# Optimization experiments

Measured on AMD Instinct MI355X. Metric: run time of the kernel, lower is better.

## Reference

```python
import jax, jax.numpy as jnp
import numpy as np

B, C, H, W = 8, 256, 128, 128
QK = 64

def setup_inputs() -> dict:
    key = jax.random.key(0)
    ks = jax.random.split(key, 8)
    s = 0.02
    return {
        "x": jax.random.normal(ks[0], (B, C, H, W), dtype=jnp.float32),
        "wq": jax.random.normal(ks[1], (QK, C), dtype=jnp.float32) * s,
        "bq": jax.random.normal(ks[2], (QK,), dtype=jnp.float32) * s,
        "wk": jax.random.normal(ks[3], (QK, C), dtype=jnp.float32) * s,
        "bk": jax.random.normal(ks[4], (QK,), dtype=jnp.float32) * s,
        "wv": jax.random.normal(ks[5], (C, C), dtype=jnp.float32) * s,
        "bv": jax.random.normal(ks[6], (C,), dtype=jnp.float32) * s,
        "gamma": jax.random.normal(ks[7], (1,), dtype=jnp.float32) * 0.1,
    }

def reference(x, wq, bq, wk, bk, wv, bv, gamma):
    # 1x1 convs == per-pixel linear projections over channels
    Q = jnp.einsum('bchw,oc->bohw', x, wq) + bq[None, :, None, None]  # (b,qk,h,w)
    K = jnp.einsum('bchw,oc->bohw', x, wk) + bk[None, :, None, None]  # (b,qk,h,w)
    V = jnp.einsum('bchw,oc->bohw', x, wv) + bv[None, :, None, None]  # (b,c,h,w)
    # row attention: for each (b,h) row, scores over width pairs
    scores = jnp.einsum('bchw,bchv->bhwv', Q, K)          # (b,h,w_q,w_k)
    attn = jax.nn.softmax(scores, axis=-1)                # softmax over keys (dim=2 after bmm)
    out = jnp.einsum('bchv,bhwv->bchw', V, attn)          # (b,c,h,w)
    return gamma[0] * out + x
```

## Files before the change

### kernel.cpp

```cpp
#include <hip/hip_runtime.h>
#include <hip/hip_bf16.h>


typedef short bf16x8 __attribute__((ext_vector_type(8)));
typedef float f32x4 __attribute__((ext_vector_type(4)));
using u32 = unsigned int;
using u16 = unsigned short;

#define XT_OFF   0
#define XT_SB    528
#define QT_OFF   67584
#define KT_OFF   86016
#define QK_SB    144
#define PL_OFF   67584
#define PL_SB    272
#define WP_OFF   104448
#define VL_OFF   141312
#define VL_SB    272
#define SMP_OFF  141312
#define BIAS_OFF 158720
#define LDS_TOTAL 160256

#define WS_WQK   0
#define WS_WV    73728

__device__ __forceinline__ u16 bfbits(float f) {
    __hip_bfloat16 h = __float2bfloat16(f);
    u16 u; __builtin_memcpy(&u, &h, 2); return u;
}
__device__ __forceinline__ u32 packbf2(float a, float b) {
    return (u32)bfbits(a) | ((u32)bfbits(b) << 16);
}
__device__ __forceinline__ float bf2f(u16 u) {
    union { u32 i; float f; } v; v.i = ((u32)u) << 16; return v.f;
}

__device__ __forceinline__ void gl2lds16(const char* g, const char* l) {
    __builtin_amdgcn_global_load_lds(
        (const __attribute__((address_space(1))) void*)(unsigned long long)g,
        (__attribute__((address_space(3))) void*)(u32)(unsigned long long)l,
        16, 0, 0);
}
__device__ __forceinline__ void stage18k(const char* g, const char* lds, int w, int l) {
    gl2lds16(g + w * 1024 + l * 16, lds + w * 1024);
    if (l < 8) gl2lds16(g + 16384 + w * 128 + l * 16, lds + 16384 + w * 128);
}
__device__ __forceinline__ void stage36k(const char* g, const char* lds, int w, int l) {
    gl2lds16(g + w * 1024 + l * 16,         lds + w * 1024);
    gl2lds16(g + 16384 + w * 1024 + l * 16, lds + 16384 + w * 1024);
    if (l < 16) gl2lds16(g + 32768 + w * 256 + l * 16, lds + 32768 + w * 256);
}

#define GATE(WAITSTR) do { \
    __builtin_amdgcn_sched_barrier(0); \
    asm volatile(WAITSTR "\n\ts_barrier" ::: "memory"); \
    __builtin_amdgcn_sched_barrier(0); \
} while (0)

__device__ __forceinline__ void hard_barrier() {
    __builtin_amdgcn_sched_barrier(0);
    asm volatile("s_barrier" ::: "memory");
    __builtin_amdgcn_sched_barrier(0);
}
__device__ __forceinline__ void lgkm_barrier() {
    __builtin_amdgcn_sched_barrier(0);
    asm volatile("s_waitcnt lgkmcnt(0)\n\ts_barrier" ::: "memory");
    __builtin_amdgcn_sched_barrier(0);
}
__device__ __forceinline__ void pin() { __builtin_amdgcn_sched_barrier(0); }

__global__ void prep_weights(const float* __restrict__ wq, const float* __restrict__ wk,
                             const float* __restrict__ wv, u32* __restrict__ ws) {
    int i = blockIdx.x * 256 + threadIdx.x;
    if (i >= 55296) return;
    u32 v = 0;
    if (i < 18432) {
        int c = i / 2304, rem = i % 2304;
        int row = rem / 36, iw = rem % 36;
        int kc = c >> 1;
        const float* m = (c & 1) ? wk : wq;
        if (iw < 32) {
            int col = kc * 64 + iw * 2;
            v = packbf2(m[row * 256 + col], m[row * 256 + col + 1]);
        }
    } else {
        int j = i - 18432;
        int c = j / 2304, rem = j % 2304;
        int row = rem / 36, iw = rem % 36;
        int mc = c >> 2, kc = c & 3;
        if (iw < 32) {
            int col = kc * 64 + iw * 2;
            v = packbf2(wv[(mc * 64 + row) * 256 + col], wv[(mc * 64 + row) * 256 + col + 1]);
        }
    }
    ws[i] = v;
}

__global__ __launch_bounds__(1024, 4) void rowattn_mfma(
    const float* __restrict__ x,
    const float* __restrict__ bq,
    const float* __restrict__ bk,
    const float* __restrict__ bv,
    const float* __restrict__ gamma,
    const char* __restrict__ wsp,
    float* __restrict__ out)
{
    __shared__ __align__(16) char smem[LDS_TOTAL];
    const int t  = threadIdx.x;
    const int l  = t & 63;
    const int a  = l & 15;
    const int q  = l >> 4;
    const int wid = __builtin_amdgcn_readfirstlane(t >> 6);
    const int mi = wid >> 2;
    const int nj = wid & 3;
    const int w0 = nj * 32;

    const int blk = blockIdx.x;
    const int b   = blk >> 5;
    const int h0  = (blk & 31) * 4;

    const char* wqk_g = wsp + WS_WQK;
    const char* wv_g  = wsp + WS_WV;
    const float g = gamma[0];

    stage18k(wqk_g,         smem + WP_OFF,         wid, l);
    stage18k(wqk_g + 18432, smem + WP_OFF + 18432, wid, l);
    pin();

    float* biasl = (float*)(smem + BIAS_OFF);
    if (t < 384) {
        float v;
        if (t < 64) v = bq[t];
        else if (t < 128) v = bk[t - 64];
        else v = bv[t - 128];
        biasl[t] = v;
    }

    const int xw  = ((wid & 8) << 3) + l;
    const int xcb = (wid & 7) * 4;
    const float* xbase = x + (size_t)(b * 256 + xcb) * 16384 + xw;
    float xv[32];
    {
        const float* xp = xbase + h0 * 128;
#pragma unroll
        for (int p = 0; p < 8; ++p)
#pragma unroll
            for (int j = 0; j < 4; ++j)
                xv[p * 4 + j] = xp[(p * 32 + j) * 16384];
    }
    pin();

#pragma unroll 1
    for (int r = 0; r < 4; ++r) {
        const int h = h0 + r;
        if (r) lgkm_barrier();

#pragma unroll
        for (int p = 0; p < 8; ++p) {
            uint2 pk;
            pk.x = packbf2(xv[p * 4 + 0], xv[p * 4 + 1]);
            pk.y = packbf2(xv[p * 4 + 2], xv[p * 4 + 3]);
            *(uint2*)(smem + XT_OFF + xw * XT_SB + (xcb + p * 32) * 2) = pk;
        }
        GATE("s_waitcnt vmcnt(8) lgkmcnt(0)");

        f32x4 accQ[2], accK[2];
        {
            f32x4 cq, ck;
#pragma unroll
            for (int rr = 0; rr < 4; ++rr) {
                cq[rr] = biasl[mi * 16 + q * 4 + rr];
                ck[rr] = biasl[64 + mi * 16 + q * 4 + rr];
            }
            accQ[0] = cq; accQ[1] = cq; accK[0] = ck; accK[1] = ck;
        }
#pragma unroll
        for (int kc = 0; kc < 4; ++kc) {
            if (kc == 2) GATE("s_waitcnt vmcnt(2)");
            if (kc == 3) GATE("s_waitcnt vmcnt(0)");
            const char* wqp = smem + WP_OFF + (kc & 1) * 18432;
            const char* wkp = wqp + 9216;
#pragma unroll
            for (int ks = 0; ks < 2; ++ks) {
                bf16x8 aq = *(const bf16x8*)(wqp + (mi * 16 + a) * 144 + ks * 64 + q * 16);
                bf16x8 ak = *(const bf16x8*)(wkp + (mi * 16 + a) * 144 + ks * 64 + q * 16);
#pragma unroll
                for (int nt = 0; nt < 2; ++nt) {
                    bf16x8 bx = *(const bf16x8*)(smem + XT_OFF + (w0 + nt * 16 + a) * XT_SB + (kc * 64 + ks * 32) * 2 + q * 16);
                    accQ[nt] = __builtin_amdgcn_mfma_f32_16x16x32_bf16(aq, bx, accQ[nt], 0, 0, 0);
                    accK[nt] = __builtin_amdgcn_mfma_f32_16x16x32_bf16(ak, bx, accK[nt], 0, 0, 0);
                }
            }
            if (kc == 0) { hard_barrier(); stage18k(wqk_g + 2 * 18432, smem + WP_OFF,         wid, l); pin(); }
            if (kc == 1) { hard_barrier(); stage18k(wqk_g + 3 * 18432, smem + WP_OFF + 18432, wid, l); pin(); }
        }
#pragma unroll
        for (int nt = 0; nt < 2; ++nt) {
            const int wrow = w0 + nt * 16 + a;
            uint2 pq; pq.x = packbf2(accQ[nt][0], accQ[nt][1]); pq.y = packbf2(accQ[nt][2], accQ[nt][3]);
            *(uint2*)(smem + QT_OFF + wrow * QK_SB + (mi * 16 + q * 4) * 2) = pq;
            uint2 pk; pk.x = packbf2(accK[nt][0], accK[nt][1]); pk.y = packbf2(accK[nt][2], accK[nt][3]);
            *(uint2*)(smem + KT_OFF + wrow * QK_SB + (mi * 16 + q * 4) * 2) = pk;
        }
        GATE("s_waitcnt lgkmcnt(0)");
        stage36k(wv_g, smem + WP_OFF, wid, l);
        pin();

        f32x4 st[2][2];
#pragma unroll
        for (int mt2 = 0; mt2 < 2; ++mt2)
#pragma unroll
            for (int nt = 0; nt < 2; ++nt) st[mt2][nt] = (f32x4){0.f, 0.f, 0.f, 0.f};
#pragma unroll
        for (int ks = 0; ks < 2; ++ks) {
            bf16x8 bq0 = *(const bf16x8*)(smem + QT_OFF + (w0 + a) * QK_SB + ks * 64 + q * 16);
            bf16x8 bq1 = *(const bf16x8*)(smem + QT_OFF + (w0 + 16 + a) * QK_SB + ks * 64 + q * 16);
            bf16x8 ak0 = *(const bf16x8*)(smem + KT_OFF + (mi * 32 + a) * QK_SB + ks * 64 + q * 16);
            bf16x8 ak1 = *(const bf16x8*)(smem + KT_OFF + (mi * 32 + 16 + a) * QK_SB + ks * 64 + q * 16);
            st[0][0] = __builtin_amdgcn_mfma_f32_16x16x32_bf16(ak0, bq0, st[0][0], 0, 0, 0);
            st[0][1] = __builtin_amdgcn_mfma_f32_16x16x32_bf16(ak0, bq1, st[0][1], 0, 0, 0);
            st[1][0] = __builtin_amdgcn_mfma_f32_16x16x32_bf16(ak1, bq0, st[1][0], 0, 0, 0);
            st[1][1] = __builtin_amdgcn_mfma_f32_16x16x32_bf16(ak1, bq1, st[1][1], 0, 0, 0);
        }
        {
            float pmax[2], psum[2];
#pragma unroll
            for (int nt = 0; nt < 2; ++nt) {
                float mx = -3.0e38f;
#pragma unroll
                for (int mt2 = 0; mt2 < 2; ++mt2)
#pragma unroll
                    for (int rr = 0; rr < 4; ++rr) mx = fmaxf(mx, st[mt2][nt][rr]);
                mx = fmaxf(mx, __shfl_xor(mx, 16, 64));
                mx = fmaxf(mx, __shfl_xor(mx, 32, 64));
                float s = 0.f;
#pragma unroll
                for (int mt2 = 0; mt2 < 2; ++mt2)
#pragma unroll
                    for (int rr = 0; rr < 4; ++rr) {
                        float e = __expf(st[mt2][nt][rr] - mx); st[mt2][nt][rr] = e; s += e;
                    }
                s += __shfl_xor(s, 16, 64);
                s += __shfl_xor(s, 32, 64);
                pmax[nt] = mx; psum[nt] = s;
            }
            float2* smp = (float2*)(smem + SMP_OFF);
            if (q == 0) {
#pragma unroll
                for (int nt = 0; nt < 2; ++nt)
                    smp[(w0 + nt * 16 + a) * 4 + mi] = make_float2(pmax[nt], psum[nt]);
            }
            lgkm_barrier();
            float f[2];
#pragma unroll
            for (int nt = 0; nt < 2; ++nt) {
                const int wq = w0 + nt * 16 + a;
                float2 pp0 = smp[wq * 4 + 0], pp1 = smp[wq * 4 + 1];
                float2 pp2 = smp[wq * 4 + 2], pp3 = smp[wq * 4 + 3];
                float m = fmaxf(fmaxf(pp0.x, pp1.x), fmaxf(pp2.x, pp3.x));
                float s = pp0.y * __expf(pp0.x - m) + pp1.y * __expf(pp1.x - m)
                        + pp2.y * __expf(pp2.x - m) + pp3.y * __expf(pp3.x - m);
                f[nt] = __expf(pmax[nt] - m) / s;
            }
#pragma unroll
            for (int nt = 0; nt < 2; ++nt) {
                const int wq = w0 + nt * 16 + a;
#pragma unroll
                for (int mt2 = 0; mt2 < 2; ++mt2) {
                    uint2 pp;
                    pp.x = packbf2(st[mt2][nt][0] * f[nt], st[mt2][nt][1] * f[nt]);
                    pp.y = packbf2(st[mt2][nt][2] * f[nt], st[mt2][nt][3] * f[nt]);
                    *(uint2*)(smem + PL_OFF + wq * PL_SB + (mi * 32 + mt2 * 16 + q * 4) * 2) = pp;
                }
            }
        }

#pragma unroll 1
        for (int mc = 0; mc < 4; ++mc) {
            if (mc == 0)              GATE("s_waitcnt vmcnt(0) lgkmcnt(0)");
            else if (mc < 3)          GATE("s_waitcnt vmcnt(8) lgkmcnt(0)");
            else if (r < 3)           GATE("s_waitcnt vmcnt(40) lgkmcnt(0)");
            else                      GATE("s_waitcnt vmcnt(8) lgkmcnt(0)");
            f32x4 accV[2];
            {
                f32x4 cv;
#pragma unroll
                for (int rr = 0; rr < 4; ++rr) cv[rr] = biasl[128 + mc * 64 + mi * 16 + q * 4 + rr];
                accV[0] = cv; accV[1] = cv;
            }
#pragma unroll
            for (int kc = 0; kc < 4; ++kc) {
                const char* wvp = smem + WP_OFF + kc * 9216;
#pragma unroll
                for (int ks = 0; ks < 2; ++ks) {
                    bf16x8 av = *(const bf16x8*)(wvp + (mi * 16 + a) * 144 + ks * 64 + q * 16);
#pragma unroll
                    for (int nt = 0; nt < 2; ++nt) {
                        bf16x8 bx = *(const bf16x8*)(smem + XT_OFF + (w0 + nt * 16 + a) * XT_SB + (kc * 64 + ks * 32) * 2 + q * 16);
                        accV[nt] = __builtin_amdgcn_mfma_f32_16x16x32_bf16(av, bx, accV[nt], 0, 0, 0);
                    }
                }
            }
#pragma unroll
            for (int nt = 0; nt < 2; ++nt)
#pragma unroll
                for (int rr = 0; rr < 4; ++rr)
                    *(u16*)(smem + VL_OFF + (mi * 16 + q * 4 + rr) * VL_SB + (w0 + nt * 16 + a) * 2) = bfbits(accV[nt][rr]);
            GATE("s_waitcnt lgkmcnt(0)");
            if (mc < 3) {
                stage36k(wv_g + (mc + 1) * 36864, smem + WP_OFF, wid, l);
                pin();
                if (mc == 2 && r < 3) {
                    const float* xn = xbase + (h + 1) * 128;
#pragma unroll
                    for (int p = 0; p < 8; ++p)
#pragma unroll
                        for (int j = 0; j < 4; ++j)
                            xv[p * 4 + j] = xn[(p * 32 + j) * 16384];
                    pin();
                }
            } else if (r < 3) {
                stage18k(wqk_g,         smem + WP_OFF,         wid, l);
                stage18k(wqk_g + 18432, smem + WP_OFF + 18432, wid, l);
                pin();
            }
            f32x4 accO[2];
            accO[0] = (f32x4){0.f, 0.f, 0.f, 0.f};
            accO[1] = (f32x4){0.f, 0.f, 0.f, 0.f};
#pragma unroll
            for (int ks = 0; ks < 4; ++ks) {
                bf16x8 av = *(const bf16x8*)(smem + VL_OFF + (mi * 16 + a) * VL_SB + ks * 64 + q * 16);
#pragma unroll
                for (int nt = 0; nt < 2; ++nt) {
                    bf16x8 bp = *(const bf16x8*)(smem + PL_OFF + (w0 + nt * 16 + a) * PL_SB + ks * 64 + q * 16);
                    accO[nt] = __builtin_amdgcn_mfma_f32_16x16x32_bf16(av, bp, accO[nt], 0, 0, 0);
                }
            }
            uint2 xp4[2];
#pragma unroll
            for (int nt = 0; nt < 2; ++nt)
                xp4[nt] = *(const uint2*)(smem + XT_OFF + (w0 + nt * 16 + a) * XT_SB + (mc * 64 + mi * 16 + q * 4) * 2);
#pragma unroll
            for (int rr = 0; rr < 4; ++rr) {
                const int c = mc * 64 + mi * 16 + q * 4 + rr;
                float* orow = out + ((b * 256 + c) * 128 + h) * 128;
#pragma unroll
                for (int nt = 0; nt < 2; ++nt) {
                    const int w = w0 + nt * 16 + a;
                    u32 word = (rr & 2) ? xp4[nt].y : xp4[nt].x;
                    u16 xvr = (rr & 1) ? (u16)(word >> 16) : (u16)(word & 0xffff);
                    orow[w] = g * accO[nt][rr] + bf2f(xvr);
                }
            }
        }
    }
}

extern "C" void kernel_launch(void* const* d_in, const int* in_sizes, int n_in,
                              void* d_out, int out_size, void* d_ws, size_t ws_size,
                              hipStream_t stream) {
    const float* x     = (const float*)d_in[0];
    const float* wq    = (const float*)d_in[1];
    const float* bq    = (const float*)d_in[2];
    const float* wk    = (const float*)d_in[3];
    const float* bk    = (const float*)d_in[4];
    const float* wv    = (const float*)d_in[5];
    const float* bv    = (const float*)d_in[6];
    const float* gamma = (const float*)d_in[7];
    float* out = (float*)d_out;

    hipLaunchKernelGGL(prep_weights, dim3(216), dim3(256), 0, stream, wq, wk, wv, (u32*)d_ws);
    hipLaunchKernelGGL(rowattn_mfma, dim3(256), dim3(1024), 0, stream,
                       x, bq, bk, bv, gamma, (const char*)d_ws, out);
}
```

Before: 359.8 us.

## Launch one block per image row instead of four pipelined rows per block

New measurement: 295.4 us. 17.9% less time.

```diff
diff --git a/kernel.cpp b/kernel.cpp
--- a/kernel.cpp
+++ b/kernel.cpp
@@ -96,7 +96,7 @@
     ws[i] = v;
 }
 
-__global__ __launch_bounds__(1024, 4) void rowattn_mfma(
+__global__ __launch_bounds__(1024, 1) void rowattn_mfma(
     const float* __restrict__ x,
     const float* __restrict__ bq,
     const float* __restrict__ bk,
@@ -115,9 +115,9 @@
     const int nj = wid & 3;
     const int w0 = nj * 32;
 
-    const int blk = blockIdx.x;
-    const int b   = blk >> 5;
-    const int h0  = (blk & 31) * 4;
+    const int bh = blockIdx.x;
+    const int b  = bh >> 7;
+    const int h  = bh & 127;
 
     const char* wqk_g = wsp + WS_WQK;
     const char* wv_g  = wsp + WS_WV;
@@ -135,35 +135,29 @@
         else v = bv[t - 128];
         biasl[t] = v;
     }
+    pin();
 
     const int xw  = ((wid & 8) << 3) + l;
     const int xcb = (wid & 7) * 4;
-    const float* xbase = x + (size_t)(b * 256 + xcb) * 16384 + xw;
+    const float* xp = x + (size_t)(b * 256 + xcb) * 16384 + (size_t)h * 128 + xw;
     float xv[32];
+#pragma unroll
+    for (int p = 0; p < 8; ++p)
+#pragma unroll
+        for (int j = 0; j < 4; ++j)
+            xv[p * 4 + j] = xp[(p * 32 + j) * 16384];
+    pin();
+
+#pragma unroll
+    for (int p = 0; p < 8; ++p) {
+        uint2 pk;
+        pk.x = packbf2(xv[p * 4 + 0], xv[p * 4 + 1]);
+        pk.y = packbf2(xv[p * 4 + 2], xv[p * 4 + 3]);
+        *(uint2*)(smem + XT_OFF + xw * XT_SB + (xcb + p * 32) * 2) = pk;
+    }
+    GATE("s_waitcnt lgkmcnt(0)");
+
     {
-        const float* xp = xbase + h0 * 128;
-#pragma unroll
-        for (int p = 0; p < 8; ++p)
-#pragma unroll
-            for (int j = 0; j < 4; ++j)
-                xv[p * 4 + j] = xp[(p * 32 + j) * 16384];
-    }
-    pin();
-
-#pragma unroll 1
-    for (int r = 0; r < 4; ++r) {
-        const int h = h0 + r;
-        if (r) lgkm_barrier();
-
-#pragma unroll
-        for (int p = 0; p < 8; ++p) {
-            uint2 pk;
-            pk.x = packbf2(xv[p * 4 + 0], xv[p * 4 + 1]);
-            pk.y = packbf2(xv[p * 4 + 2], xv[p * 4 + 3]);
-            *(uint2*)(smem + XT_OFF + xw * XT_SB + (xcb + p * 32) * 2) = pk;
-        }
-        GATE("s_waitcnt vmcnt(8) lgkmcnt(0)");
-
         f32x4 accQ[2], accK[2];
         {
             f32x4 cq, ck;
@@ -202,155 +196,140 @@
             uint2 pk; pk.x = packbf2(accK[nt][0], accK[nt][1]); pk.y = packbf2(accK[nt][2], accK[nt][3]);
             *(uint2*)(smem + KT_OFF + wrow * QK_SB + (mi * 16 + q * 4) * 2) = pk;
         }
+    }
+    GATE("s_waitcnt lgkmcnt(0)");
+    stage36k(wv_g, smem + WP_OFF, wid, l);
+    pin();
+
+    f32x4 st[2][2];
+#pragma unroll
+    for (int mt2 = 0; mt2 < 2; ++mt2)
+#pragma unroll
+        for (int nt = 0; nt < 2; ++nt) st[mt2][nt] = (f32x4){0.f, 0.f, 0.f, 0.f};
+#pragma unroll
+    for (int ks = 0; ks < 2; ++ks) {
+        bf16x8 bq0 = *(const bf16x8*)(smem + QT_OFF + (w0 + a) * QK_SB + ks * 64 + q * 16);
+        bf16x8 bq1 = *(const bf16x8*)(smem + QT_OFF + (w0 + 16 + a) * QK_SB + ks * 64 + q * 16);
+        bf16x8 ak0 = *(const bf16x8*)(smem + KT_OFF + (mi * 32 + a) * QK_SB + ks * 64 + q * 16);
+        bf16x8 ak1 = *(const bf16x8*)(smem + KT_OFF + (mi * 32 + 16 + a) * QK_SB + ks * 64 + q * 16);
+        st[0][0] = __builtin_amdgcn_mfma_f32_16x16x32_bf16(ak0, bq0, st[0][0], 0, 0, 0);
+        st[0][1] = __builtin_amdgcn_mfma_f32_16x16x32_bf16(ak0, bq1, st[0][1], 0, 0, 0);
+        st[1][0] = __builtin_amdgcn_mfma_f32_16x16x32_bf16(ak1, bq0, st[1][0], 0, 0, 0);
+        st[1][1] = __builtin_amdgcn_mfma_f32_16x16x32_bf16(ak1, bq1, st[1][1], 0, 0, 0);
+    }
+    {
+        float pmax[2], psum[2];
+#pragma unroll
+        for (int nt = 0; nt < 2; ++nt) {
+            float mx = -3.0e38f;
+#pragma unroll
+            for (int mt2 = 0; mt2 < 2; ++mt2)
+#pragma unroll
+                for (int rr = 0; rr < 4; ++rr) mx = fmaxf(mx, st[mt2][nt][rr]);
+            mx = fmaxf(mx, __shfl_xor(mx, 16, 64));
+            mx = fmaxf(mx, __shfl_xor(mx, 32, 64));
+            float s = 0.f;
+#pragma unroll
+            for (int mt2 = 0; mt2 < 2; ++mt2)
+#pragma unroll
+                for (int rr = 0; rr < 4; ++rr) {
+                    float e = __expf(st[mt2][nt][rr] - mx); st[mt2][nt][rr] = e; s += e;
+                }
+            s += __shfl_xor(s, 16, 64);
+            s += __shfl_xor(s, 32, 64);
+            pmax[nt] = mx; psum[nt] = s;
+        }
+        float2* smp = (float2*)(smem + SMP_OFF);
+        if (q == 0) {
+#pragma unroll
+            for (int nt = 0; nt < 2; ++nt)
+                smp[(w0 + nt * 16 + a) * 4 + mi] = make_float2(pmax[nt], psum[nt]);
+        }
+        lgkm_barrier();
+        float f[2];
+#pragma unroll
+        for (int nt = 0; nt < 2; ++nt) {
+            const int wq = w0 + nt * 16 + a;
+            float2 pp0 = smp[wq * 4 + 0], pp1 = smp[wq * 4 + 1];
+            float2 pp2 = smp[wq * 4 + 2], pp3 = smp[wq * 4 + 3];
+            float m = fmaxf(fmaxf(pp0.x, pp1.x), fmaxf(pp2.x, pp3.x));
+            float s = pp0.y * __expf(pp0.x - m) + pp1.y * __expf(pp1.x - m)
+                    + pp2.y * __expf(pp2.x - m) + pp3.y * __expf(pp3.x - m);
+            f[nt] = __expf(pmax[nt] - m) / s;
+        }
+#pragma unroll
+        for (int nt = 0; nt < 2; ++nt) {
+            const int wq = w0 + nt * 16 + a;
+#pragma unroll
+            for (int mt2 = 0; mt2 < 2; ++mt2) {
+                uint2 pp;
+                pp.x = packbf2(st[mt2][nt][0] * f[nt], st[mt2][nt][1] * f[nt]);
+                pp.y = packbf2(st[mt2][nt][2] * f[nt], st[mt2][nt][3] * f[nt]);
+                *(uint2*)(smem + PL_OFF + wq * PL_SB + (mi * 32 + mt2 * 16 + q * 4) * 2) = pp;
+            }
+        }
+    }
+
+#pragma unroll 1
+    for (int mc = 0; mc < 4; ++mc) {
+        if (mc == 0) GATE("s_waitcnt vmcnt(0) lgkmcnt(0)");
+        else         GATE("s_waitcnt vmcnt(8) lgkmcnt(0)");
+        f32x4 accV[2];
+        {
+            f32x4 cv;
+#pragma unroll
+            for (int rr = 0; rr < 4; ++rr) cv[rr] = biasl[128 + mc * 64 + mi * 16 + q * 4 + rr];
+            accV[0] = cv; accV[1] = cv;
+        }
+#pragma unroll
+        for (int kc = 0; kc < 4; ++kc) {
+            const char* wvp = smem + WP_OFF + kc * 9216;
+#pragma unroll
+            for (int ks = 0; ks < 2; ++ks) {
+                bf16x8 av = *(const bf16x8*)(wvp + (mi * 16 + a) * 144 + ks * 64 + q * 16);
+#pragma unroll
+                for (int nt = 0; nt < 2; ++nt) {
+                    bf16x8 bx = *(const bf16x8*)(smem + XT_OFF + (w0 + nt * 16 + a) * XT_SB + (kc * 64 + ks * 32) * 2 + q * 16);
+                    accV[nt] = __builtin_amdgcn_mfma_f32_16x16x32_bf16(av, bx, accV[nt], 0, 0, 0);
+                }
+            }
+        }
+#pragma unroll
+        for (int nt = 0; nt < 2; ++nt)
+#pragma unroll
+            for (int rr = 0; rr < 4; ++rr)
+                *(u16*)(smem + VL_OFF + (mi * 16 + q * 4 + rr) * VL_SB + (w0 + nt * 16 + a) * 2) = bfbits(accV[nt][rr]);
         GATE("s_waitcnt lgkmcnt(0)");
-        stage36k(wv_g, smem + WP_OFF, wid, l);
-        pin();
-
-        f32x4 st[2][2];
-#pragma unroll
-        for (int mt2 = 0; mt2 < 2; ++mt2)
-#pragma unroll
-            for (int nt = 0; nt < 2; ++nt) st[mt2][nt] = (f32x4){0.f, 0.f, 0.f, 0.f};
-#pragma unroll
-        for (int ks = 0; ks < 2; ++ks) {
-            bf16x8 bq0 = *(const bf16x8*)(smem + QT_OFF + (w0 + a) * QK_SB + ks * 64 + q * 16);
-            bf16x8 bq1 = *(const bf16x8*)(smem + QT_OFF + (w0 + 16 + a) * QK_SB + ks * 64 + q * 16);
-            bf16x8 ak0 = *(const bf16x8*)(smem + KT_OFF + (mi * 32 + a) * QK_SB + ks * 64 + q * 16);
-            bf16x8 ak1 = *(const bf16x8*)(smem + KT_OFF + (mi * 32 + 16 + a) * QK_SB + ks * 64 + q * 16);
-            st[0][0] = __builtin_amdgcn_mfma_f32_16x16x32_bf16(ak0, bq0, st[0][0], 0, 0, 0);
-            st[0][1] = __builtin_amdgcn_mfma_f32_16x16x32_bf16(ak0, bq1, st[0][1], 0, 0, 0);
-            st[1][0] = __builtin_amdgcn_mfma_f32_16x16x32_bf16(ak1, bq0, st[1][0], 0, 0, 0);
-            st[1][1] = __builtin_amdgcn_mfma_f32_16x16x32_bf16(ak1, bq1, st[1][1], 0, 0, 0);
-        }
-        {
-            float pmax[2], psum[2];
+        if (mc < 3) {
+            stage36k(wv_g + (mc + 1) * 36864, smem + WP_OFF, wid, l);
+            pin();
+        }
+        f32x4 accO[2];
+        accO[0] = (f32x4){0.f, 0.f, 0.f, 0.f};
+        accO[1] = (f32x4){0.f, 0.f, 0.f, 0.f};
+#pragma unroll
+        for (int ks = 0; ks < 4; ++ks) {
+            bf16x8 av = *(const bf16x8*)(smem + VL_OFF + (mi * 16 + a) * VL_SB + ks * 64 + q * 16);
 #pragma unroll
             for (int nt = 0; nt < 2; ++nt) {
-                float mx = -3.0e38f;
-#pragma unroll
-                for (int mt2 = 0; mt2 < 2; ++mt2)
-#pragma unroll
-                    for (int rr = 0; rr < 4; ++rr) mx = fmaxf(mx, st[mt2][nt][rr]);
-                mx = fmaxf(mx, __shfl_xor(mx, 16, 64));
-                mx = fmaxf(mx, __shfl_xor(mx, 32, 64));
-                float s = 0.f;
-#pragma unroll
-                for (int mt2 = 0; mt2 < 2; ++mt2)
-#pragma unroll
-                    for (int rr = 0; rr < 4; ++rr) {
-                        float e = __expf(st[mt2][nt][rr] - mx); st[mt2][nt][rr] = e; s += e;
-                    }
-                s += __shfl_xor(s, 16, 64);
-                s += __shfl_xor(s, 32, 64);
-                pmax[nt] = mx; psum[nt] = s;
-            }
-            float2* smp = (float2*)(smem + SMP_OFF);
-            if (q == 0) {
-#pragma unroll
-                for (int nt = 0; nt < 2; ++nt)
-                    smp[(w0 + nt * 16 + a) * 4 + mi] = make_float2(pmax[nt], psum[nt]);
-            }
-            lgkm_barrier();
-            float f[2];
+                bf16x8 bp = *(const bf16x8*)(smem + PL_OFF + (w0 + nt * 16 + a) * PL_SB + ks * 64 + q * 16);
+                accO[nt] = __builtin_amdgcn_mfma_f32_16x16x32_bf16(av, bp, accO[nt], 0, 0, 0);
+            }
+        }
+        uint2 xp4[2];
+#pragma unroll
+        for (int nt = 0; nt < 2; ++nt)
+            xp4[nt] = *(const uint2*)(smem + XT_OFF + (w0 + nt * 16 + a) * XT_SB + (mc * 64 + mi * 16 + q * 4) * 2);
+#pragma unroll
+        for (int rr = 0; rr < 4; ++rr) {
+            const int c = mc * 64 + mi * 16 + q * 4 + rr;
+            float* orow = out + ((b * 256 + c) * 128 + h) * 128;
 #pragma unroll
             for (int nt = 0; nt < 2; ++nt) {
-                const int wq = w0 + nt * 16 + a;
-                float2 pp0 = smp[wq * 4 + 0], pp1 = smp[wq * 4 + 1];
-                float2 pp2 = smp[wq * 4 + 2], pp3 = smp[wq * 4 + 3];
-                float m = fmaxf(fmaxf(pp0.x, pp1.x), fmaxf(pp2.x, pp3.x));
-                float s = pp0.y * __expf(pp0.x - m) + pp1.y * __expf(pp1.x - m)
-                        + pp2.y * __expf(pp2.x - m) + pp3.y * __expf(pp3.x - m);
-                f[nt] = __expf(pmax[nt] - m) / s;
-            }
-#pragma unroll
-            for (int nt = 0; nt < 2; ++nt) {
-                const int wq = w0 + nt * 16 + a;
-#pragma unroll
-                for (int mt2 = 0; mt2 < 2; ++mt2) {
-                    uint2 pp;
-                    pp.x = packbf2(st[mt2][nt][0] * f[nt], st[mt2][nt][1] * f[nt]);
-                    pp.y = packbf2(st[mt2][nt][2] * f[nt], st[mt2][nt][3] * f[nt]);
-                    *(uint2*)(smem + PL_OFF + wq * PL_SB + (mi * 32 + mt2 * 16 + q * 4) * 2) = pp;
-                }
-            }
-        }
-
-#pragma unroll 1
-        for (int mc = 0; mc < 4; ++mc) {
-            if (mc == 0)              GATE("s_waitcnt vmcnt(0) lgkmcnt(0)");
-            else if (mc < 3)          GATE("s_waitcnt vmcnt(8) lgkmcnt(0)");
-            else if (r < 3)           GATE("s_waitcnt vmcnt(40) lgkmcnt(0)");
-            else                      GATE("s_waitcnt vmcnt(8) lgkmcnt(0)");
-            f32x4 accV[2];
-            {
-                f32x4 cv;
-#pragma unroll
-                for (int rr = 0; rr < 4; ++rr) cv[rr] = biasl[128 + mc * 64 + mi * 16 + q * 4 + rr];
-                accV[0] = cv; accV[1] = cv;
-            }
-#pragma unroll
-            for (int kc = 0; kc < 4; ++kc) {
-                const char* wvp = smem + WP_OFF + kc * 9216;
-#pragma unroll
-                for (int ks = 0; ks < 2; ++ks) {
-                    bf16x8 av = *(const bf16x8*)(wvp + (mi * 16 + a) * 144 + ks * 64 + q * 16);
-#pragma unroll
-                    for (int nt = 0; nt < 2; ++nt) {
-                        bf16x8 bx = *(const bf16x8*)(smem + XT_OFF + (w0 + nt * 16 + a) * XT_SB + (kc * 64 + ks * 32) * 2 + q * 16);
-                        accV[nt] = __builtin_amdgcn_mfma_f32_16x16x32_bf16(av, bx, accV[nt], 0, 0, 0);
-                    }
-                }
-            }
-#pragma unroll
-            for (int nt = 0; nt < 2; ++nt)
-#pragma unroll
-                for (int rr = 0; rr < 4; ++rr)
-                    *(u16*)(smem + VL_OFF + (mi * 16 + q * 4 + rr) * VL_SB + (w0 + nt * 16 + a) * 2) = bfbits(accV[nt][rr]);
-            GATE("s_waitcnt lgkmcnt(0)");
-            if (mc < 3) {
-                stage36k(wv_g + (mc + 1) * 36864, smem + WP_OFF, wid, l);
-                pin();
-                if (mc == 2 && r < 3) {
-                    const float* xn = xbase + (h + 1) * 128;
-#pragma unroll
-                    for (int p = 0; p < 8; ++p)
-#pragma unroll
-                        for (int j = 0; j < 4; ++j)
-                            xv[p * 4 + j] = xn[(p * 32 + j) * 16384];
-                    pin();
-                }
-            } else if (r < 3) {
-                stage18k(wqk_g,         smem + WP_OFF,         wid, l);
-                stage18k(wqk_g + 18432, smem + WP_OFF + 18432, wid, l);
-                pin();
-            }
-            f32x4 accO[2];
-            accO[0] = (f32x4){0.f, 0.f, 0.f, 0.f};
-            accO[1] = (f32x4){0.f, 0.f, 0.f, 0.f};
-#pragma unroll
-            for (int ks = 0; ks < 4; ++ks) {
-                bf16x8 av = *(const bf16x8*)(smem + VL_OFF + (mi * 16 + a) * VL_SB + ks * 64 + q * 16);
-#pragma unroll
-                for (int nt = 0; nt < 2; ++nt) {
-                    bf16x8 bp = *(const bf16x8*)(smem + PL_OFF + (w0 + nt * 16 + a) * PL_SB + ks * 64 + q * 16);
-                    accO[nt] = __builtin_amdgcn_mfma_f32_16x16x32_bf16(av, bp, accO[nt], 0, 0, 0);
-                }
-            }
-            uint2 xp4[2];
-#pragma unroll
-            for (int nt = 0; nt < 2; ++nt)
-                xp4[nt] = *(const uint2*)(smem + XT_OFF + (w0 + nt * 16 + a) * XT_SB + (mc * 64 + mi * 16 + q * 4) * 2);
-#pragma unroll
-            for (int rr = 0; rr < 4; ++rr) {
-                const int c = mc * 64 + mi * 16 + q * 4 + rr;
-                float* orow = out + ((b * 256 + c) * 128 + h) * 128;
-#pragma unroll
-                for (int nt = 0; nt < 2; ++nt) {
-                    const int w = w0 + nt * 16 + a;
-                    u32 word = (rr & 2) ? xp4[nt].y : xp4[nt].x;
-                    u16 xvr = (rr & 1) ? (u16)(word >> 16) : (u16)(word & 0xffff);
-                    orow[w] = g * accO[nt][rr] + bf2f(xvr);
-                }
+                const int w = w0 + nt * 16 + a;
+                u32 word = (rr & 2) ? xp4[nt].y : xp4[nt].x;
+                u16 xvr = (rr & 1) ? (u16)(word >> 16) : (u16)(word & 0xffff);
+                orow[w] = g * accO[nt][rr] + bf2f(xvr);
             }
         }
     }
@@ -370,6 +349,6 @@
     float* out = (float*)d_out;
 
     hipLaunchKernelGGL(prep_weights, dim3(216), dim3(256), 0, stream, wq, wk, wv, (u32*)d_ws);
-    hipLaunchKernelGGL(rowattn_mfma, dim3(256), dim3(1024), 0, stream,
+    hipLaunchKernelGGL(rowattn_mfma, dim3(1024), dim3(1024), 0, stream,
                        x, bq, bk, bv, gamma, (const char*)d_ws, out);
 }
```
